# Kernel tuning notes

Hardware: AMD Instinct MI355X
Metric: run time of the kernel (lower is better)

Reference implementation:

```python
import jax, jax.numpy as jnp
import numpy as np

B, S, IN, OUT = 4, 2048, 4096, 4096


def setup_inputs() -> dict:
    key = jax.random.key(0)
    k1, k2 = jax.random.split(key, 2)
    x = jax.random.normal(k1, (B, S, IN), dtype=jnp.float32)
    # Materialize the quantized weight the way bitsandbytes int8_vectorwise_quant does:
    # per-output-row absmax (SCB) and int8 codes CB = round(W * 127 / absmax_row).
    Wf = jax.random.normal(k2, (OUT, IN), dtype=jnp.float32) * 0.02
    absmax = jnp.max(jnp.abs(Wf), axis=1)  # [OUT]
    CB = jnp.round(Wf * (127.0 / absmax)[:, None]).astype(jnp.int8)  # [OUT, IN]
    SCB = absmax.astype(jnp.float32)  # [OUT], per-row absmax scale
    return {"x": x, "CB": CB, "SCB": SCB}


def reference(x, CB, SCB):
    # LLM.int8()-style forward (has_fp16_weights=False, no outlier split needed for
    # well-behaved activations): dynamic row-wise int8 quantization of x, int8 GEMM
    # accumulated in int32, then dequant by (absmax_x/127) * (SCB/127).
    absmax_x = jnp.max(jnp.abs(x), axis=-1, keepdims=True)  # [B,S,1]
    sx = absmax_x / 127.0
    xq = jnp.round(x / sx).astype(jnp.int8)  # [B,S,IN]
    acc = jnp.einsum("bsk,ok->bso", xq, CB, preferred_element_type=jnp.int32)
    y = acc.astype(jnp.float32) * sx * (SCB / 127.0)[None, None, :]  # [B,S,OUT]
    return y
```

## Files before the change

### kernel.cpp

```cpp
#include <hip/hip_runtime.h>
#include <stdint.h>

static constexpr int Mtot = 8192;
static constexpr int Ntot = 4096;
static constexpr int Ktot = 4096;

using i32x4 = __attribute__((ext_vector_type(4))) int;

#define GLD16(gptr, lptr)                                                                   \
  __builtin_amdgcn_global_load_lds((const __attribute__((address_space(1))) void*)(gptr),   \
                                   (__attribute__((address_space(3))) void*)(lptr), 16, 0, 0)

__global__ __launch_bounds__(256) void prep_kernel(const int* __restrict__ cb32,
                                                   int8_t* __restrict__ cb8,
                                                   const float* __restrict__ x,
                                                   int8_t* __restrict__ xq,
                                                   float* __restrict__ sx) {
  __shared__ float wmax[4];
  if (blockIdx.x < 16384) {
    const int idx = blockIdx.x * 256 + threadIdx.x;
    const int4 v = reinterpret_cast<const int4*>(cb32)[idx];
    const unsigned packed = (unsigned)(v.x & 0xff) | ((unsigned)(v.y & 0xff) << 8) |
                            ((unsigned)(v.z & 0xff) << 16) | ((unsigned)(v.w & 0xff) << 24);
    reinterpret_cast<unsigned*>(cb8)[idx] = packed;
    return;
  }
  const int row = blockIdx.x - 16384;
  const float4* xr = reinterpret_cast<const float4*>(x + (size_t)row * Ktot);
  float4 v[4];
  float am = 0.f;
#pragma unroll
  for (int i = 0; i < 4; ++i) {
    v[i] = xr[threadIdx.x + i * 256];
    am = fmaxf(am, fmaxf(fmaxf(fabsf(v[i].x), fabsf(v[i].y)),
                         fmaxf(fabsf(v[i].z), fabsf(v[i].w))));
  }
#pragma unroll
  for (int off = 32; off > 0; off >>= 1) am = fmaxf(am, __shfl_xor(am, off));
  if ((threadIdx.x & 63) == 0) wmax[threadIdx.x >> 6] = am;
  __syncthreads();
  am = fmaxf(fmaxf(wmax[0], wmax[1]), fmaxf(wmax[2], wmax[3]));
  const float inv = 127.0f / am;
  if (threadIdx.x == 0) sx[row] = am * (1.0f / 127.0f);
  unsigned* dq = reinterpret_cast<unsigned*>(xq + (size_t)row * Ktot);
#pragma unroll
  for (int i = 0; i < 4; ++i) {
    const int q0 = (int)rintf(v[i].x * inv);
    const int q1 = (int)rintf(v[i].y * inv);
    const int q2 = (int)rintf(v[i].z * inv);
    const int q3 = (int)rintf(v[i].w * inv);
    dq[threadIdx.x + i * 256] = (unsigned)(q0 & 0xff) | ((unsigned)(q1 & 0xff) << 8) |
                                ((unsigned)(q2 & 0xff) << 16) | ((unsigned)(q3 & 0xff) << 24);
  }
}

__global__ __launch_bounds__(512, 2) void gemm_i8_kernel(const int8_t* __restrict__ A,
                                                         const int8_t* __restrict__ B,
                                                         const float* __restrict__ sx,
                                                         const float* __restrict__ scb,
                                                         float* __restrict__ C) {
  constexpr int BK = 128;
  constexpr int NT = Ktot / BK;
  __shared__ __align__(16) int8_t lds[131072];

  const int tid = threadIdx.x;
  const int lane = tid & 63;
  const int wid = tid >> 6;

  const int wg = (int)blockIdx.x;
  const int wgs = (wg & 7) * 64 + (wg >> 3);
  const int m0 = (wgs >> 4) * 256;
  const int n0 = (wgs & 15) * 256;

  const int wm = (wid >> 2) * 128;
  const int wn = (wid & 3) * 64;

  const int srow = tid >> 3;
  const int scol = ((tid & 7) * 16) ^ ((srow & 7) << 4);
  const int8_t* gA = A + (size_t)(m0 + srow) * Ktot + scol;
  const int8_t* gB = B + (size_t)(n0 + srow) * Ktot + scol;

  const int l15 = lane & 15;
  const int lc0 = ((lane >> 4) * 16) ^ ((lane & 7) << 4);
  const int aOff = (wm + l15) * 128 + lc0;
  const int bOff = 65536 + (wn + l15) * 128 + lc0;

  i32x4 acc[8][4];
#pragma unroll
  for (int f = 0; f < 8; ++f)
#pragma unroll
    for (int g = 0; g < 4; ++g) acc[f][g] = (i32x4)0;

#pragma unroll
  for (int i = 0; i < 4; ++i) {
    GLD16(gA + (size_t)(i * 64) * Ktot, &lds[i * 8192 + tid * 16]);
    GLD16(gB + (size_t)(i * 64) * Ktot, &lds[65536 + i * 8192 + tid * 16]);
  }
  __syncthreads();

#pragma unroll 2
  for (int t = 0; t < NT; ++t) {
    const int bo = (t & 1) * 32768;
    const int so = ((t & 1) ^ 1) * 32768;
    i32x4 a[4], b[4];

#pragma unroll
    for (int f = 0; f < 4; ++f) a[f] = *(const i32x4*)&lds[bo + aOff + f * 2048];
#pragma unroll
    for (int g = 0; g < 4; ++g) b[g] = *(const i32x4*)&lds[bo + bOff + g * 2048];
    if (t + 1 < NT) {
      const size_t kn = (size_t)(t + 1) * BK;
#pragma unroll
      for (int i = 0; i < 4; ++i) {
        GLD16(gA + kn + (size_t)(i * 64) * Ktot, &lds[so + i * 8192 + tid * 16]);
        GLD16(gB + kn + (size_t)(i * 64) * Ktot, &lds[65536 + so + i * 8192 + tid * 16]);
      }
    }
    __builtin_amdgcn_s_barrier();
    __builtin_amdgcn_s_setprio(1);
#pragma unroll
    for (int f = 0; f < 4; ++f)
#pragma unroll
      for (int g = 0; g < 4; ++g)
        acc[f][g] = __builtin_amdgcn_mfma_i32_16x16x64_i8(a[f], b[g], acc[f][g], 0, 0, 0);
    __builtin_amdgcn_s_setprio(0);
    __builtin_amdgcn_s_barrier();

#pragma unroll
    for (int f = 0; f < 4; ++f) a[f] = *(const i32x4*)&lds[bo + aOff + (f + 4) * 2048];
    __builtin_amdgcn_s_barrier();
    __builtin_amdgcn_s_setprio(1);
#pragma unroll
    for (int f = 0; f < 4; ++f)
#pragma unroll
      for (int g = 0; g < 4; ++g)
        acc[f + 4][g] = __builtin_amdgcn_mfma_i32_16x16x64_i8(a[f], b[g], acc[f + 4][g], 0, 0, 0);
    __builtin_amdgcn_s_setprio(0);
    __builtin_amdgcn_s_barrier();

#pragma unroll
    for (int f = 0; f < 4; ++f) a[f] = *(const i32x4*)&lds[bo + (aOff ^ 64) + f * 2048];
#pragma unroll
    for (int g = 0; g < 4; ++g) b[g] = *(const i32x4*)&lds[bo + (bOff ^ 64) + g * 2048];
    __builtin_amdgcn_s_barrier();
    __builtin_amdgcn_s_setprio(1);
#pragma unroll
    for (int f = 0; f < 4; ++f)
#pragma unroll
      for (int g = 0; g < 4; ++g)
        acc[f][g] = __builtin_amdgcn_mfma_i32_16x16x64_i8(a[f], b[g], acc[f][g], 0, 0, 0);
    __builtin_amdgcn_s_setprio(0);
    __builtin_amdgcn_s_barrier();

#pragma unroll
    for (int f = 0; f < 4; ++f) a[f] = *(const i32x4*)&lds[bo + (aOff ^ 64) + (f + 4) * 2048];
    __builtin_amdgcn_s_barrier();
    __builtin_amdgcn_s_setprio(1);
#pragma unroll
    for (int f = 0; f < 4; ++f)
#pragma unroll
      for (int g = 0; g < 4; ++g)
        acc[f + 4][g] = __builtin_amdgcn_mfma_i32_16x16x64_i8(a[f], b[g], acc[f + 4][g], 0, 0, 0);
    __builtin_amdgcn_s_setprio(0);
    __syncthreads();
  }

  const int col = lane & 15;
  const int rbase = (lane >> 4) * 4;
#pragma unroll
  for (int f = 0; f < 8; ++f) {
    const int gmb = m0 + wm + f * 16 + rbase;
    float sm[4];
#pragma unroll
    for (int r = 0; r < 4; ++r) sm[r] = sx[gmb + r];
#pragma unroll
    for (int g = 0; g < 4; ++g) {
      const int gn = n0 + wn + g * 16 + col;
      const float snv = scb[gn] * (1.0f / 127.0f);
#pragma unroll
      for (int r = 0; r < 4; ++r)
        C[(size_t)(gmb + r) * Ntot + gn] = (float)acc[f][g][r] * sm[r] * snv;
    }
  }
}

extern "C" void kernel_launch(void* const* d_in, const int* in_sizes, int n_in,
                              void* d_out, int out_size, void* d_ws, size_t ws_size,
                              hipStream_t stream) {
  const float* x = (const float*)d_in[0];
  const int* CB32 = (const int*)d_in[1];
  const float* SCB = (const float*)d_in[2];
  float* out = (float*)d_out;

  int8_t* xq = (int8_t*)d_ws;
  int8_t* cb8 = (int8_t*)d_ws + (size_t)Mtot * Ktot;
  float* sx = (float*)((int8_t*)d_ws + (size_t)Mtot * Ktot + (size_t)Ntot * Ktot);

  prep_kernel<<<16384 + Mtot, 256, 0, stream>>>(CB32, cb8, x, xq, sx);
  gemm_i8_kernel<<<512, 512, 0, stream>>>(xq, cb8, sx, SCB, out);
}
```

Before: 386.0 us.

## Split next-tile prefetch across phases with fine-grained vmcnt waits and peeled tail

The GEMM main loop now issues the next K-tile's B loads in the first phase and the A loads in the third phase, instead of all at once. Explicit s_waitcnt vmcnt counts plus plain barriers replace the full __syncthreads at the end of each iteration. The last iteration is peeled so the loop body needs no conditional prefetch. This aims to spread global-to-LDS traffic across the MFMA phases and stop draining every outstanding load at each barrier. In exchange, correctness now depends on the hand-counted vmcnt values matching the compiler's actual load ordering.

```diff
diff --git a/kernel.cpp b/kernel.cpp
--- a/kernel.cpp
+++ b/kernel.cpp
@@ -10,6 +10,7 @@
 #define GLD16(gptr, lptr)                                                                   \
   __builtin_amdgcn_global_load_lds((const __attribute__((address_space(1))) void*)(gptr),   \
                                    (__attribute__((address_space(3))) void*)(lptr), 16, 0, 0)
+#define WAITVM(N) asm volatile("s_waitcnt vmcnt(" #N ")" ::: "memory")
 
 __global__ __launch_bounds__(256) void prep_kernel(const int* __restrict__ cb32,
                                                    int8_t* __restrict__ cb8,
@@ -92,38 +93,36 @@
     for (int g = 0; g < 4; ++g) acc[f][g] = (i32x4)0;
 
 #pragma unroll
-  for (int i = 0; i < 4; ++i) {
-    GLD16(gA + (size_t)(i * 64) * Ktot, &lds[i * 8192 + tid * 16]);
-    GLD16(gB + (size_t)(i * 64) * Ktot, &lds[65536 + i * 8192 + tid * 16]);
-  }
-  __syncthreads();
-
-#pragma unroll 2
-  for (int t = 0; t < NT; ++t) {
+  for (int i = 0; i < 4; ++i) GLD16(gB + (size_t)(i * 64) * Ktot, &lds[65536 + i * 8192 + tid * 16]);
+  GLD16(gA + (size_t)(0 * 64) * Ktot, &lds[0 * 8192 + tid * 16]);
+  GLD16(gA + (size_t)(2 * 64) * Ktot, &lds[2 * 8192 + tid * 16]);
+  GLD16(gA + (size_t)(1 * 64) * Ktot, &lds[1 * 8192 + tid * 16]);
+  GLD16(gA + (size_t)(3 * 64) * Ktot, &lds[3 * 8192 + tid * 16]);
+  WAITVM(2);
+  __builtin_amdgcn_s_barrier();
+
+  for (int t = 0; t < NT - 1; ++t) {
     const int bo = (t & 1) * 32768;
-    const int so = ((t & 1) ^ 1) * 32768;
+    const int so = bo ^ 32768;
+    const size_t kn = (size_t)(t + 1) * BK;
     i32x4 a[4], b[4];
 
 #pragma unroll
     for (int f = 0; f < 4; ++f) a[f] = *(const i32x4*)&lds[bo + aOff + f * 2048];
 #pragma unroll
     for (int g = 0; g < 4; ++g) b[g] = *(const i32x4*)&lds[bo + bOff + g * 2048];
-    if (t + 1 < NT) {
-      const size_t kn = (size_t)(t + 1) * BK;
-#pragma unroll
-      for (int i = 0; i < 4; ++i) {
-        GLD16(gA + kn + (size_t)(i * 64) * Ktot, &lds[so + i * 8192 + tid * 16]);
-        GLD16(gB + kn + (size_t)(i * 64) * Ktot, &lds[65536 + so + i * 8192 + tid * 16]);
-      }
-    }
-    __builtin_amdgcn_s_barrier();
-    __builtin_amdgcn_s_setprio(1);
-#pragma unroll
-    for (int f = 0; f < 4; ++f)
-#pragma unroll
-      for (int g = 0; g < 4; ++g)
-        acc[f][g] = __builtin_amdgcn_mfma_i32_16x16x64_i8(a[f], b[g], acc[f][g], 0, 0, 0);
-    __builtin_amdgcn_s_setprio(0);
+#pragma unroll
+    for (int i = 0; i < 4; ++i)
+      GLD16(gB + kn + (size_t)(i * 64) * Ktot, &lds[65536 + so + i * 8192 + tid * 16]);
+    __builtin_amdgcn_s_barrier();
+    __builtin_amdgcn_s_setprio(1);
+#pragma unroll
+    for (int f = 0; f < 4; ++f)
+#pragma unroll
+      for (int g = 0; g < 4; ++g)
+        acc[f][g] = __builtin_amdgcn_mfma_i32_16x16x64_i8(a[f], b[g], acc[f][g], 0, 0, 0);
+    __builtin_amdgcn_s_setprio(0);
+    WAITVM(4);
     __builtin_amdgcn_s_barrier();
 
 #pragma unroll
@@ -142,6 +141,10 @@
     for (int f = 0; f < 4; ++f) a[f] = *(const i32x4*)&lds[bo + (aOff ^ 64) + f * 2048];
 #pragma unroll
     for (int g = 0; g < 4; ++g) b[g] = *(const i32x4*)&lds[bo + (bOff ^ 64) + g * 2048];
+    GLD16(gA + kn + (size_t)(0 * 64) * Ktot, &lds[so + 0 * 8192 + tid * 16]);
+    GLD16(gA + kn + (size_t)(2 * 64) * Ktot, &lds[so + 2 * 8192 + tid * 16]);
+    GLD16(gA + kn + (size_t)(1 * 64) * Ktot, &lds[so + 1 * 8192 + tid * 16]);
+    GLD16(gA + kn + (size_t)(3 * 64) * Ktot, &lds[so + 3 * 8192 + tid * 16]);
     __builtin_amdgcn_s_barrier();
     __builtin_amdgcn_s_setprio(1);
 #pragma unroll
@@ -162,7 +165,63 @@
       for (int g = 0; g < 4; ++g)
         acc[f + 4][g] = __builtin_amdgcn_mfma_i32_16x16x64_i8(a[f], b[g], acc[f + 4][g], 0, 0, 0);
     __builtin_amdgcn_s_setprio(0);
-    __syncthreads();
+    WAITVM(2);
+    __builtin_amdgcn_s_barrier();
+  }
+
+  {
+    const int bo = ((NT - 1) & 1) * 32768;
+    i32x4 a[4], b[4];
+#pragma unroll
+    for (int f = 0; f < 4; ++f) a[f] = *(const i32x4*)&lds[bo + aOff + f * 2048];
+#pragma unroll
+    for (int g = 0; g < 4; ++g) b[g] = *(const i32x4*)&lds[bo + bOff + g * 2048];
+    __builtin_amdgcn_s_barrier();
+    __builtin_amdgcn_s_setprio(1);
+#pragma unroll
+    for (int f = 0; f < 4; ++f)
+#pragma unroll
+      for (int g = 0; g < 4; ++g)
+        acc[f][g] = __builtin_amdgcn_mfma_i32_16x16x64_i8(a[f], b[g], acc[f][g], 0, 0, 0);
+    __builtin_amdgcn_s_setprio(0);
+    WAITVM(0);
+    __builtin_amdgcn_s_barrier();
+
+#pragma unroll
+    for (int f = 0; f < 4; ++f) a[f] = *(const i32x4*)&lds[bo + aOff + (f + 4) * 2048];
+    __builtin_amdgcn_s_barrier();
+    __builtin_amdgcn_s_setprio(1);
+#pragma unroll
+    for (int f = 0; f < 4; ++f)
+#pragma unroll
+      for (int g = 0; g < 4; ++g)
+        acc[f + 4][g] = __builtin_amdgcn_mfma_i32_16x16x64_i8(a[f], b[g], acc[f + 4][g], 0, 0, 0);
+    __builtin_amdgcn_s_setprio(0);
+    __builtin_amdgcn_s_barrier();
+
+#pragma unroll
+    for (int f = 0; f < 4; ++f) a[f] = *(const i32x4*)&lds[bo + (aOff ^ 64) + f * 2048];
+#pragma unroll
+    for (int g = 0; g < 4; ++g) b[g] = *(const i32x4*)&lds[bo + (bOff ^ 64) + g * 2048];
+    __builtin_amdgcn_s_barrier();
+    __builtin_amdgcn_s_setprio(1);
+#pragma unroll
+    for (int f = 0; f < 4; ++f)
+#pragma unroll
+      for (int g = 0; g < 4; ++g)
+        acc[f][g] = __builtin_amdgcn_mfma_i32_16x16x64_i8(a[f], b[g], acc[f][g], 0, 0, 0);
+    __builtin_amdgcn_s_setprio(0);
+    __builtin_amdgcn_s_barrier();
+
+#pragma unroll
+    for (int f = 0; f < 4; ++f) a[f] = *(const i32x4*)&lds[bo + (aOff ^ 64) + (f + 4) * 2048];
+    __builtin_amdgcn_s_setprio(1);
+#pragma unroll
+    for (int f = 0; f < 4; ++f)
+#pragma unroll
+      for (int g = 0; g < 4; ++g)
+        acc[f + 4][g] = __builtin_amdgcn_mfma_i32_16x16x64_i8(a[f], b[g], acc[f + 4][g], 0, 0, 0);
+    __builtin_amdgcn_s_setprio(0);
   }
 
   const int col = lane & 15;
```

Measured after the change: 385.3 us. About the same (-0.2%).

## Use 16-wave workgroups with register-prefetched LDS fragments and vmcnt-based pipelining

Applied to the files above, without the earlier changes.

The GEMM block grows from 512 to 1024 threads, so each wave now owns a 64x64 tile instead of 128x64, which halves the accumulator registers per wave. The main loop is rewritten as a software pipeline: B and A fragments for the next phase are read from LDS while MFMAs on the current ones run, and explicit s_waitcnt vmcnt plus barriers replace the per-phase __syncthreads. The aim is more waves to hide latency and less barrier stall. In exchange, register pressure under launch_bounds(1024,4) may cause spills, and the hand-placed waitcnt and barrier ordering could introduce LDS races.

```diff
diff --git a/kernel.cpp b/kernel.cpp
--- a/kernel.cpp
+++ b/kernel.cpp
@@ -10,6 +10,8 @@
 #define GLD16(gptr, lptr)                                                                   \
   __builtin_amdgcn_global_load_lds((const __attribute__((address_space(1))) void*)(gptr),   \
                                    (__attribute__((address_space(3))) void*)(lptr), 16, 0, 0)
+#define WAITVM(N) asm volatile("s_waitcnt vmcnt(" #N ")" ::: "memory")
+#define MFMA16(a, b, c) __builtin_amdgcn_mfma_i32_16x16x64_i8((a), (b), (c), 0, 0, 0)
 
 __global__ __launch_bounds__(256) void prep_kernel(const int* __restrict__ cb32,
                                                    int8_t* __restrict__ cb8,
@@ -54,13 +56,14 @@
   }
 }
 
-__global__ __launch_bounds__(512, 2) void gemm_i8_kernel(const int8_t* __restrict__ A,
-                                                         const int8_t* __restrict__ B,
-                                                         const float* __restrict__ sx,
-                                                         const float* __restrict__ scb,
-                                                         float* __restrict__ C) {
+__global__ __launch_bounds__(1024, 4) void gemm_i8_kernel(const int8_t* __restrict__ A,
+                                                          const int8_t* __restrict__ B,
+                                                          const float* __restrict__ sx,
+                                                          const float* __restrict__ scb,
+                                                          float* __restrict__ C) {
   constexpr int BK = 128;
   constexpr int NT = Ktot / BK;
+  constexpr size_t ROWS128 = (size_t)128 * Ktot;
   __shared__ __align__(16) int8_t lds[131072];
 
   const int tid = threadIdx.x;
@@ -72,7 +75,7 @@
   const int m0 = (wgs >> 4) * 256;
   const int n0 = (wgs & 15) * 256;
 
-  const int wm = (wid >> 2) * 128;
+  const int wm = (wid >> 2) * 64;
   const int wn = (wid & 3) * 64;
 
   const int srow = tid >> 3;
@@ -85,90 +88,122 @@
   const int aOff = (wm + l15) * 128 + lc0;
   const int bOff = 65536 + (wn + l15) * 128 + lc0;
 
-  i32x4 acc[8][4];
-#pragma unroll
-  for (int f = 0; f < 8; ++f)
+  i32x4 acc[4][4];
+#pragma unroll
+  for (int f = 0; f < 4; ++f)
 #pragma unroll
     for (int g = 0; g < 4; ++g) acc[f][g] = (i32x4)0;
 
-#pragma unroll
-  for (int i = 0; i < 4; ++i) {
-    GLD16(gA + (size_t)(i * 64) * Ktot, &lds[i * 8192 + tid * 16]);
-    GLD16(gB + (size_t)(i * 64) * Ktot, &lds[65536 + i * 8192 + tid * 16]);
-  }
-  __syncthreads();
-
-#pragma unroll 2
-  for (int t = 0; t < NT; ++t) {
+  i32x4 aH[4], aN[4], bA[2], bB[2], bC[2], bD[2];
+
+  GLD16(gA, &lds[tid * 16]);
+  GLD16(gA + ROWS128, &lds[16384 + tid * 16]);
+  GLD16(gB, &lds[65536 + tid * 16]);
+  GLD16(gB + ROWS128, &lds[65536 + 16384 + tid * 16]);
+  WAITVM(0);
+  __builtin_amdgcn_s_barrier();
+#pragma unroll
+  for (int f = 0; f < 4; ++f) aH[f] = *(const i32x4*)&lds[aOff + f * 2048];
+  bA[0] = *(const i32x4*)&lds[bOff];
+  bA[1] = *(const i32x4*)&lds[bOff + 2048];
+
+  for (int t = 0; t < NT - 1; ++t) {
     const int bo = (t & 1) * 32768;
-    const int so = ((t & 1) ^ 1) * 32768;
-    i32x4 a[4], b[4];
-
-#pragma unroll
-    for (int f = 0; f < 4; ++f) a[f] = *(const i32x4*)&lds[bo + aOff + f * 2048];
-#pragma unroll
-    for (int g = 0; g < 4; ++g) b[g] = *(const i32x4*)&lds[bo + bOff + g * 2048];
-    if (t + 1 < NT) {
-      const size_t kn = (size_t)(t + 1) * BK;
-#pragma unroll
-      for (int i = 0; i < 4; ++i) {
-        GLD16(gA + kn + (size_t)(i * 64) * Ktot, &lds[so + i * 8192 + tid * 16]);
-        GLD16(gB + kn + (size_t)(i * 64) * Ktot, &lds[65536 + so + i * 8192 + tid * 16]);
-      }
-    }
+    const int so = bo ^ 32768;
+    const size_t kn = (size_t)(t + 1) * BK;
+
+    bB[0] = *(const i32x4*)&lds[bo + bOff + 2 * 2048];
+    bB[1] = *(const i32x4*)&lds[bo + bOff + 3 * 2048];
+    GLD16(gA + kn, &lds[so + tid * 16]);
+    GLD16(gA + ROWS128 + kn, &lds[so + 16384 + tid * 16]);
+    GLD16(gB + kn, &lds[65536 + so + tid * 16]);
+    GLD16(gB + ROWS128 + kn, &lds[65536 + so + 16384 + tid * 16]);
+    __builtin_amdgcn_s_setprio(1);
+#pragma unroll
+    for (int f = 0; f < 4; ++f) {
+      acc[f][0] = MFMA16(aH[f], bA[0], acc[f][0]);
+      acc[f][1] = MFMA16(aH[f], bA[1], acc[f][1]);
+    }
+    __builtin_amdgcn_s_setprio(0);
+
+    bC[0] = *(const i32x4*)&lds[bo + (bOff ^ 64)];
+    bC[1] = *(const i32x4*)&lds[bo + (bOff ^ 64) + 2048];
+    __builtin_amdgcn_s_setprio(1);
+#pragma unroll
+    for (int f = 0; f < 4; ++f) {
+      acc[f][2] = MFMA16(aH[f], bB[0], acc[f][2]);
+      acc[f][3] = MFMA16(aH[f], bB[1], acc[f][3]);
+    }
+    __builtin_amdgcn_s_setprio(0);
+
+#pragma unroll
+    for (int f = 0; f < 4; ++f) aN[f] = *(const i32x4*)&lds[bo + (aOff ^ 64) + f * 2048];
+    bD[0] = *(const i32x4*)&lds[bo + (bOff ^ 64) + 2 * 2048];
+    bD[1] = *(const i32x4*)&lds[bo + (bOff ^ 64) + 3 * 2048];
+    __builtin_amdgcn_s_setprio(1);
+#pragma unroll
+    for (int f = 0; f < 4; ++f) {
+      acc[f][0] = MFMA16(aN[f], bC[0], acc[f][0]);
+      acc[f][1] = MFMA16(aN[f], bC[1], acc[f][1]);
+    }
+    __builtin_amdgcn_s_setprio(0);
+    WAITVM(2);
     __builtin_amdgcn_s_barrier();
-    __builtin_amdgcn_s_setprio(1);
-#pragma unroll
-    for (int f = 0; f < 4; ++f)
-#pragma unroll
-      for (int g = 0; g < 4; ++g)
-        acc[f][g] = __builtin_amdgcn_mfma_i32_16x16x64_i8(a[f], b[g], acc[f][g], 0, 0, 0);
-    __builtin_amdgcn_s_setprio(0);
+
+#pragma unroll
+    for (int f = 0; f < 4; ++f) aH[f] = *(const i32x4*)&lds[so + aOff + f * 2048];
+    __builtin_amdgcn_s_setprio(1);
+#pragma unroll
+    for (int f = 0; f < 4; ++f) {
+      acc[f][2] = MFMA16(aN[f], bD[0], acc[f][2]);
+      acc[f][3] = MFMA16(aN[f], bD[1], acc[f][3]);
+    }
+    __builtin_amdgcn_s_setprio(0);
+    WAITVM(0);
     __builtin_amdgcn_s_barrier();
-
-#pragma unroll
-    for (int f = 0; f < 4; ++f) a[f] = *(const i32x4*)&lds[bo + aOff + (f + 4) * 2048];
-    __builtin_amdgcn_s_barrier();
-    __builtin_amdgcn_s_setprio(1);
-#pragma unroll
-    for (int f = 0; f < 4; ++f)
-#pragma unroll
-      for (int g = 0; g < 4; ++g)
-        acc[f + 4][g] = __builtin_amdgcn_mfma_i32_16x16x64_i8(a[f], b[g], acc[f + 4][g], 0, 0, 0);
-    __builtin_amdgcn_s_setprio(0);
-    __builtin_amdgcn_s_barrier();
-
-#pragma unroll
-    for (int f = 0; f < 4; ++f) a[f] = *(const i32x4*)&lds[bo + (aOff ^ 64) + f * 2048];
-#pragma unroll
-    for (int g = 0; g < 4; ++g) b[g] = *(const i32x4*)&lds[bo + (bOff ^ 64) + g * 2048];
-    __builtin_amdgcn_s_barrier();
-    __builtin_amdgcn_s_setprio(1);
-#pragma unroll
-    for (int f = 0; f < 4; ++f)
-#pragma unroll
-      for (int g = 0; g < 4; ++g)
-        acc[f][g] = __builtin_amdgcn_mfma_i32_16x16x64_i8(a[f], b[g], acc[f][g], 0, 0, 0);
-    __builtin_amdgcn_s_setprio(0);
-    __builtin_amdgcn_s_barrier();
-
-#pragma unroll
-    for (int f = 0; f < 4; ++f) a[f] = *(const i32x4*)&lds[bo + (aOff ^ 64) + (f + 4) * 2048];
-    __builtin_amdgcn_s_barrier();
-    __builtin_amdgcn_s_setprio(1);
-#pragma unroll
-    for (int f = 0; f < 4; ++f)
-#pragma unroll
-      for (int g = 0; g < 4; ++g)
-        acc[f + 4][g] = __builtin_amdgcn_mfma_i32_16x16x64_i8(a[f], b[g], acc[f + 4][g], 0, 0, 0);
-    __builtin_amdgcn_s_setprio(0);
-    __syncthreads();
+    bA[0] = *(const i32x4*)&lds[so + bOff];
+    bA[1] = *(const i32x4*)&lds[so + bOff + 2048];
+  }
+
+  {
+    const int bo = ((NT - 1) & 1) * 32768;
+    bB[0] = *(const i32x4*)&lds[bo + bOff + 2 * 2048];
+    bB[1] = *(const i32x4*)&lds[bo + bOff + 3 * 2048];
+    __builtin_amdgcn_s_setprio(1);
+#pragma unroll
+    for (int f = 0; f < 4; ++f) {
+      acc[f][0] = MFMA16(aH[f], bA[0], acc[f][0]);
+      acc[f][1] = MFMA16(aH[f], bA[1], acc[f][1]);
+    }
+    __builtin_amdgcn_s_setprio(0);
+    bC[0] = *(const i32x4*)&lds[bo + (bOff ^ 64)];
+    bC[1] = *(const i32x4*)&lds[bo + (bOff ^ 64) + 2048];
+    __builtin_amdgcn_s_setprio(1);
+#pragma unroll
+    for (int f = 0; f < 4; ++f) {
+      acc[f][2] = MFMA16(aH[f], bB[0], acc[f][2]);
+      acc[f][3] = MFMA16(aH[f], bB[1], acc[f][3]);
+    }
+    __builtin_amdgcn_s_setprio(0);
+#pragma unroll
+    for (int f = 0; f < 4; ++f) aN[f] = *(const i32x4*)&lds[bo + (aOff ^ 64) + f * 2048];
+    bD[0] = *(const i32x4*)&lds[bo + (bOff ^ 64) + 2 * 2048];
+    bD[1] = *(const i32x4*)&lds[bo + (bOff ^ 64) + 3 * 2048];
+    __builtin_amdgcn_s_setprio(1);
+#pragma unroll
+    for (int f = 0; f < 4; ++f) {
+      acc[f][0] = MFMA16(aN[f], bC[0], acc[f][0]);
+      acc[f][1] = MFMA16(aN[f], bC[1], acc[f][1]);
+      acc[f][2] = MFMA16(aN[f], bD[0], acc[f][2]);
+      acc[f][3] = MFMA16(aN[f], bD[1], acc[f][3]);
+    }
+    __builtin_amdgcn_s_setprio(0);
   }
 
   const int col = lane & 15;
   const int rbase = (lane >> 4) * 4;
 #pragma unroll
-  for (int f = 0; f < 8; ++f) {
+  for (int f = 0; f < 4; ++f) {
     const int gmb = m0 + wm + f * 16 + rbase;
     float sm[4];
 #pragma unroll
@@ -197,5 +232,5 @@
   float* sx = (float*)((int8_t*)d_ws + (size_t)Mtot * Ktot + (size_t)Ntot * Ktot);
 
   prep_kernel<<<16384 + Mtot, 256, 0, stream>>>(CB32, cb8, x, xq, sx);
-  gemm_i8_kernel<<<512, 512, 0, stream>>>(xq, cb8, sx, SCB, out);
+  gemm_i8_kernel<<<512, 1024, 0, stream>>>(xq, cb8, sx, SCB, out);
 }
```

Result: no change. 378.4 us (-2.0%).
